# Kernel tuning notes

Hardware: AMD Instinct MI355X
Metric: run time of the kernel (lower is better)

## Reference

```python
import jax, jax.numpy as jnp
import numpy as np

N_HEADS = 16
BLOCK_SIZE = 256


def setup_inputs() -> dict:
    key = jax.random.key(0)
    ks = jax.random.split(key, 5)
    B, T, C = 4, 4096, 1024
    scale = 0.02
    return {
        "x": jax.random.normal(ks[0], (B, T, C), dtype=jnp.float32),
        "Wqkv": jax.random.normal(ks[1], (C, 3 * C), dtype=jnp.float32) * scale,
        "bqkv": jnp.zeros((3 * C,), dtype=jnp.float32),
        "Wout": jax.random.normal(ks[2], (C, C), dtype=jnp.float32) * scale,
        "bout": jnp.zeros((C,), dtype=jnp.float32),
    }


def reference(x, Wqkv, bqkv, Wout, bout):
    B, T, C = x.shape
    H = N_HEADS
    hd = C // H
    bs = BLOCK_SIZE
    nb = T // bs

    qkv = x @ Wqkv + bqkv                     # [B,T,3C]
    qkv = qkv.reshape(B, T, H, 3 * hd).transpose(0, 2, 1, 3)  # [B,H,T,3hd]
    q, k, v = jnp.split(qkv, 3, axis=-1)      # each [B,H,T,hd]

    # block-diagonal local attention: reshape T -> (nb, bs)
    q = q.reshape(B, H, nb, bs, hd)
    k = k.reshape(B, H, nb, bs, hd)
    v = v.reshape(B, H, nb, bs, hd)

    scores = jnp.einsum("bhnqd,bhnkd->bhnqk", q, k) * (hd ** -0.5)
    attn = jax.nn.softmax(scores, axis=-1)
    o = jnp.einsum("bhnqk,bhnkd->bhnqd", attn, v)  # [B,H,nb,bs,hd]

    o = o.reshape(B, H, T, hd).transpose(0, 2, 1, 3).reshape(B, T, C)
    return o @ Wout + bout
```

## Files before the change

### kernel.cpp

```cpp
#include <hip/hip_runtime.h>

typedef unsigned int u32;
typedef unsigned short u16;
typedef short bf16x8 __attribute__((ext_vector_type(8)));
typedef u16 u16x8 __attribute__((ext_vector_type(8)));
typedef float f32x4 __attribute__((ext_vector_type(4)));


__device__ __forceinline__ u16 f2bf(float f) {
  unsigned u = __float_as_uint(f);
  u += 0x7FFFu + ((u >> 16) & 1u);
  return (u16)(u >> 16);
}

typedef const void __attribute__((address_space(1)))* gas_p;
typedef void __attribute__((address_space(3)))* las_p;

__device__ __forceinline__ void async_ld16(const void* g, void* l) {
  __builtin_amdgcn_global_load_lds((gas_p)g, (las_p)l, 16, 0, 0);
}


__global__ __launch_bounds__(256) void k_cvt_bf16(const float* __restrict__ in,
                                                  u16* __restrict__ out, int n8) {
  int i = blockIdx.x * 256 + threadIdx.x;
  if (i >= n8) return;
  const float4* p = (const float4*)in + (size_t)i * 2;
  float4 a = p[0], b = p[1];
  u16x8 o;
  o[0] = f2bf(a.x); o[1] = f2bf(a.y); o[2] = f2bf(a.z); o[3] = f2bf(a.w);
  o[4] = f2bf(b.x); o[5] = f2bf(b.y); o[6] = f2bf(b.z); o[7] = f2bf(b.w);
  *((u16x8*)out + i) = o;
}


__global__ __launch_bounds__(256) void k_transpose_cvt(const float* __restrict__ in,
                                                       u16* __restrict__ out,
                                                       int R, int Ncols) {
  __shared__ u16 t[32][33];
  int tx = threadIdx.x, ty = threadIdx.y;
  int c0 = blockIdx.x * 32, r0 = blockIdx.y * 32;
#pragma unroll
  for (int j = 0; j < 32; j += 8)
    t[ty + j][tx] = f2bf(in[(size_t)(r0 + ty + j) * Ncols + c0 + tx]);
  __syncthreads();
#pragma unroll
  for (int j = 0; j < 32; j += 8)
    out[(size_t)(c0 + ty + j) * R + r0 + tx] = t[tx][ty + j];
}


#define STAGE_A2(h_, src_, dd_) do {                                       \
    const u16* g_ = (src_) + (size_t)(h_) * 128 * KK;                      \
    u16* s_ = lds + (dd_) * 16384 + (((h_) * 128 + w * 16) << 6);          \
    async_ld16(g_, s_);                                                    \
    async_ld16(g_ + 8 * (size_t)KK, s_ + 512);                             \
  } while (0)

#define STAGE_B2(h_, src_, dd_) do {                                       \
    const u16* g_ = (src_) + (size_t)(h_) * 128 * KK;                      \
    u16* s_ = lds + 32768 + (dd_) * 16384 + (((h_) * 128 + w * 16) << 6);  \
    async_ld16(g_, s_);                                                    \
    async_ld16(g_ + 8 * (size_t)KK, s_ + 512);                             \
  } while (0)

#define MQUAD(M0, N0)                                                      \
    _Pragma("unroll") for (int ks = 0; ks < 2; ++ks)                       \
    _Pragma("unroll") for (int mm = 0; mm < 4; ++mm)                       \
    _Pragma("unroll") for (int nn = 0; nn < 2; ++nn)                       \
      acc[(M0) + mm][(N0) + nn] = __builtin_amdgcn_mfma_f32_16x16x32_bf16( \
          a[(M0) + mm][ks], b[(N0) + nn][ks], acc[(M0) + mm][(N0) + nn], 0, 0, 0);

#define TBX(d_, bS_, aS_)                                                  \
  {                                                                        \
    const int doA = (d_) * 16384, doB = 32768 + (d_) * 16384;              \
    _Pragma("unroll") for (int f = 0; f < 4; ++f) {                        \
      a[f][0] = *(const bf16x8*)(lds + doA + rAoff + f * 1024 + c0);       \
      a[f][1] = *(const bf16x8*)(lds + doA + rAoff + f * 1024 + c1);       \
    }                                                                      \
    _Pragma("unroll") for (int f = 0; f < 2; ++f) {                        \
      b[f][0] = *(const bf16x8*)(lds + doB + rBoff + f * 1024 + c0);       \
      b[f][1] = *(const bf16x8*)(lds + doB + rBoff + f * 1024 + c1);       \
    }                                                                      \
    STAGE_B2(0, bS_, (d_) ^ 1);                                            \
    asm volatile("s_waitcnt lgkmcnt(8)");                                  \
    __builtin_amdgcn_s_barrier();                                          \
    asm volatile("s_waitcnt lgkmcnt(0)");                                  \
    __builtin_amdgcn_s_setprio(1);                                         \
    MQUAD(0, 0)                                                            \
    __builtin_amdgcn_s_setprio(0);                                         \
    __builtin_amdgcn_s_barrier();                                          \
    _Pragma("unroll") for (int f = 4; f < 8; ++f) {                        \
      a[f][0] = *(const bf16x8*)(lds + doA + rAoff + f * 1024 + c0);       \
      a[f][1] = *(const bf16x8*)(lds + doA + rAoff + f * 1024 + c1);       \
    }                                                                      \
    STAGE_B2(1, bS_, (d_) ^ 1);                                            \
    __builtin_amdgcn_s_barrier();                                          \
    asm volatile("s_waitcnt lgkmcnt(0)");                                  \
    __builtin_amdgcn_s_setprio(1);                                         \
    MQUAD(4, 0)                                                            \
    __builtin_amdgcn_s_setprio(0);                                         \
    __builtin_amdgcn_s_barrier();                                          \
    _Pragma("unroll") for (int f = 2; f < 4; ++f) {                        \
      b[f][0] = *(const bf16x8*)(lds + doB + rBoff + f * 1024 + c0);       \
      b[f][1] = *(const bf16x8*)(lds + doB + rBoff + f * 1024 + c1);       \
    }                                                                      \
    STAGE_A2(0, aS_, (d_));                                                \
    __builtin_amdgcn_s_barrier();                                          \
    asm volatile("s_waitcnt lgkmcnt(0)");                                  \
    __builtin_amdgcn_s_setprio(1);                                         \
    MQUAD(4, 2)                                                            \
    __builtin_amdgcn_s_setprio(0);                                         \
    __builtin_amdgcn_s_barrier();                                          \
    STAGE_A2(1, aS_, (d_));                                                \
    __builtin_amdgcn_s_setprio(1);                                         \
    MQUAD(0, 2)                                                            \
    __builtin_amdgcn_s_setprio(0);                                         \
    asm volatile("s_waitcnt vmcnt(4)");                                    \
    __builtin_amdgcn_s_barrier();                                          \
  }

#define EPI(PM0, PN0) do {                                                      \
    int ccol0 = (PN0) + wn * 64 + (lane & 15);                                  \
    float bv0 = bias[ccol0], bv1 = bias[ccol0 + 16];                            \
    float bv2 = bias[ccol0 + 32], bv3 = bias[ccol0 + 48];                       \
    size_t crow0 = (size_t)((PM0) + wm * 128 + ((lane >> 4) << 2));             \
    _Pragma("unroll") for (int m = 0; m < 8; ++m)                               \
    _Pragma("unroll") for (int reg = 0; reg < 4; ++reg) {                       \
      size_t ro = (crow0 + m * 16 + reg) * (size_t)N + ccol0;                   \
      float v0 = acc[m][0][reg] + bv0, v1 = acc[m][1][reg] + bv1;               \
      float v2 = acc[m][2][reg] + bv2, v3 = acc[m][3][reg] + bv3;               \
      if (OUT_BF16) {                                                           \
        ((u16*)Cout)[ro] = f2bf(v0); ((u16*)Cout)[ro + 16] = f2bf(v1);          \
        ((u16*)Cout)[ro + 32] = f2bf(v2); ((u16*)Cout)[ro + 48] = f2bf(v3);     \
      } else {                                                                  \
        ((float*)Cout)[ro] = v0; ((float*)Cout)[ro + 16] = v1;                  \
        ((float*)Cout)[ro + 32] = v2; ((float*)Cout)[ro + 48] = v3;             \
      }                                                                         \
    }                                                                           \
  } while (0)

#define TILE_COORD(tt, mm0, nn0) do {                                           \
    int q_ = nwg >> 3, r_ = nwg & 7, x_ = (tt) & 7, loc_ = (tt) >> 3;           \
    int swz_ = (x_ < r_ ? x_ * (q_ + 1) : r_ * (q_ + 1) + (x_ - r_) * q_) + loc_;\
    mm0 = (swz_ / nbn) << 8; nn0 = (swz_ % nbn) << 8;                           \
  } while (0)

#define ZERO_ACC do {                                                           \
    _Pragma("unroll") for (int m = 0; m < 8; ++m)                               \
    _Pragma("unroll") for (int n = 0; n < 4; ++n)                               \
      acc[m][n] = (f32x4){0.f, 0.f, 0.f, 0.f};                                  \
  } while (0)

template <int OUT_BF16, int KK>
__global__ __launch_bounds__(512, 2) void k_gemm8(const u16* __restrict__ A,
                                                  const u16* __restrict__ Bt,
                                                  const float* __restrict__ bias,
                                                  void* __restrict__ Cout,
                                                  int M, int N) {
  extern __shared__ u16 lds[];
  const int NT = KK / 64;

  int nbn = N >> 8, nbm = M >> 8, nwg = nbm * nbn;
  int tid = threadIdx.x;
  int w = tid >> 6, lane = tid & 63;
  int wm = w >> 2, wn = w & 3;

  int rAoff = (wm * 128 + (lane & 15)) << 6;
  int rBoff = (wn * 64 + (lane & 15)) << 6;
  int hi8 = (lane >> 4) << 3, key8 = (lane & 7) << 3;
  int c0 = hi8 ^ key8;
  int c1 = (32 | hi8) ^ key8;
  int rowoff = w * 16 + (lane >> 3);
  int soff = ((lane & 7) ^ (lane >> 3)) << 3;

  bf16x8 a[8][2], b[4][2];
  f32x4 acc[8][4];

  int t = blockIdx.x;
  int m0, n0;
  TILE_COORD(t, m0, n0);
  const u16* pAg = A + (size_t)(m0 + rowoff) * KK + soff;
  const u16* pBg = Bt + (size_t)(n0 + rowoff) * KK + soff;

  STAGE_A2(0, pAg, 0); STAGE_A2(1, pAg, 0);
  STAGE_B2(0, pBg, 0); STAGE_B2(1, pBg, 0);
  STAGE_A2(0, pAg + 64, 1); STAGE_A2(1, pAg + 64, 1);
  asm volatile("s_waitcnt vmcnt(4)");
  __builtin_amdgcn_s_barrier();
  ZERO_ACC;

  for (;;) {
    int tn = t + gridDim.x;
    bool last = tn >= nwg;
    const u16 *pAgN, *pBgN;
    int m0N = m0, n0N = n0;
    if (last) {
      pAgN = pAg; pBgN = pBg;
    } else {
      TILE_COORD(tn, m0N, n0N);
      pAgN = A + (size_t)(m0N + rowoff) * KK + soff;
      pBgN = Bt + (size_t)(n0N + rowoff) * KK + soff;
    }

    for (int k = 0; k < NT; k += 2) {
      const u16* bS1 = pBg + (k + 1) * 64;
      const u16* aS2 = (k + 2 < NT) ? pAg + (k + 2) * 64 : pAgN + (k + 2 - NT) * 64;
      TBX(0, bS1, aS2);
      const u16* bS2 = (k + 2 < NT) ? pBg + (k + 2) * 64 : pBgN + (k + 2 - NT) * 64;
      const u16* aS3 = (k + 3 < NT) ? pAg + (k + 3) * 64 : pAgN + (k + 3 - NT) * 64;
      TBX(1, bS2, aS3);
    }

    EPI(m0, n0);
    if (last) break;
    t = tn; m0 = m0N; n0 = n0N; pAg = pAgN; pBg = pBgN;
    ZERO_ACC;
  }
  asm volatile("s_waitcnt vmcnt(0)");
}


__global__ __launch_bounds__(512, 2) void k_attn2(const u16* __restrict__ qkv,
                                                  u16* __restrict__ o) {
  __shared__ u16 ldsK[256 * 64];
  __shared__ u16 ldsV[64 * 256];

  int bid = blockIdx.x;
  int g = ((bid & 7) << 7) | (bid >> 3);
  int blk = g & 15, h = (g >> 4) & 15, b = g >> 8;

  int tid = threadIdx.x;
  int w = tid >> 6, lane = tid & 63;
  int hgrp = lane >> 4;
  size_t rowb = ((size_t)(b * 4096 + blk * 256)) * 3072 + (size_t)h * 192;

  int qbase = w * 32;
  const u16* qp0 = qkv + rowb + (size_t)(qbase + (lane & 15)) * 3072 + hgrp * 8;
  const u16* qp1 = qp0 + (size_t)16 * 3072;
  bf16x8 qf00 = *(const bf16x8*)(qp0);
  bf16x8 qf01 = *(const bf16x8*)(qp0 + 32);
  bf16x8 qf10 = *(const bf16x8*)(qp1);
  bf16x8 qf11 = *(const bf16x8*)(qp1 + 32);

#pragma unroll
  for (int it = 0; it < 4; ++it) {
    int trow = it * 64 + (tid >> 3);
    const u16* ksrc = qkv + rowb + (size_t)trow * 3072 + 64 +
                      (((lane & 7) ^ (lane >> 3)) << 3);
    async_ld16(ksrc, ldsK + (it * 64 + w * 8) * 64);
    int d0 = (tid & 7) << 3;
    uint4 vv = *(const uint4*)(qkv + rowb + (size_t)trow * 3072 + 128 + d0);
    union { uint4 v; u16 s[8]; } uv;
    uv.v = vv;
#pragma unroll
    for (int j = 0; j < 8; ++j) {
      int d = d0 + j;
      int key = (((d & 7) ^ ((d >> 3) & 7)) & 7) << 4;
      *(u16*)((char*)ldsV + d * 512 + ((2 * trow) ^ key)) = uv.s[j];
    }
  }
  __syncthreads();

  f32x4 acc0[16] = {}, acc1[16] = {};
  int cb = hgrp << 4;
#pragma unroll
  for (int ct = 0; ct < 16; ++ct) {
    int krow = ct * 16 + (lane & 15);
    const char* kb = (const char*)ldsK + krow * 128;
    int key = (krow & 7) << 4;
    bf16x8 k0 = *(const bf16x8*)(kb + (cb ^ key));
    bf16x8 k1 = *(const bf16x8*)(kb + ((64 + cb) ^ key));
    acc0[ct] = __builtin_amdgcn_mfma_f32_16x16x32_bf16(k0, qf00, acc0[ct], 0, 0, 0);
    acc0[ct] = __builtin_amdgcn_mfma_f32_16x16x32_bf16(k1, qf01, acc0[ct], 0, 0, 0);
    acc1[ct] = __builtin_amdgcn_mfma_f32_16x16x32_bf16(k0, qf10, acc1[ct], 0, 0, 0);
    acc1[ct] = __builtin_amdgcn_mfma_f32_16x16x32_bf16(k1, qf11, acc1[ct], 0, 0, 0);
  }

  const float SC = 0.125f * 1.44269504f;
  float rden0, rden1;
  {
    float mx = -1e30f;
#pragma unroll
    for (int ct = 0; ct < 16; ++ct)
#pragma unroll
      for (int rg = 0; rg < 4; ++rg) mx = fmaxf(mx, acc0[ct][rg]);
    mx = fmaxf(mx, __shfl_xor(mx, 16));
    mx = fmaxf(mx, __shfl_xor(mx, 32));
    float s = 0.f;
#pragma unroll
    for (int ct = 0; ct < 16; ++ct)
#pragma unroll
      for (int rg = 0; rg < 4; ++rg) {
        float p = exp2f((acc0[ct][rg] - mx) * SC);
        acc0[ct][rg] = p;
        s += p;
      }
    s += __shfl_xor(s, 16);
    s += __shfl_xor(s, 32);
    rden0 = 1.f / s;
  }
  {
    float mx = -1e30f;
#pragma unroll
    for (int ct = 0; ct < 16; ++ct)
#pragma unroll
      for (int rg = 0; rg < 4; ++rg) mx = fmaxf(mx, acc1[ct][rg]);
    mx = fmaxf(mx, __shfl_xor(mx, 16));
    mx = fmaxf(mx, __shfl_xor(mx, 32));
    float s = 0.f;
#pragma unroll
    for (int ct = 0; ct < 16; ++ct)
#pragma unroll
      for (int rg = 0; rg < 4; ++rg) {
        float p = exp2f((acc1[ct][rg] - mx) * SC);
        acc1[ct][rg] = p;
        s += p;
      }
    s += __shfl_xor(s, 16);
    s += __shfl_xor(s, 32);
    rden1 = 1.f / s;
  }

  int s1 = (lane & 15) + ((lane >> 4) & 1) * 32;
  int s2 = s1 + 16;
  bool lo = (lane < 32);
  bf16x8 pa0[8], pa1[8];
#define PCONV(ACC, PA)                                                      \
  _Pragma("unroll") for (int kt = 0; kt < 8; ++kt) {                        \
    u32 wA0, wB0, wA1, wB1;                                                 \
    asm("v_cvt_pk_bf16_f32 %0, %1, %2" : "=v"(wA0)                          \
        : "v"(ACC[2 * kt][0]), "v"(ACC[2 * kt][1]));                        \
    asm("v_cvt_pk_bf16_f32 %0, %1, %2" : "=v"(wB0)                          \
        : "v"(ACC[2 * kt][2]), "v"(ACC[2 * kt][3]));                        \
    asm("v_cvt_pk_bf16_f32 %0, %1, %2" : "=v"(wA1)                          \
        : "v"(ACC[2 * kt + 1][0]), "v"(ACC[2 * kt + 1][1]));                \
    asm("v_cvt_pk_bf16_f32 %0, %1, %2" : "=v"(wB1)                          \
        : "v"(ACC[2 * kt + 1][2]), "v"(ACC[2 * kt + 1][3]));                \
    u32 t0a = (u32)__shfl((int)wA0, s1), t0b = (u32)__shfl((int)wA1, s1);   \
    u32 t1a = (u32)__shfl((int)wB0, s1), t1b = (u32)__shfl((int)wB1, s1);   \
    u32 t2a = (u32)__shfl((int)wA0, s2), t2b = (u32)__shfl((int)wA1, s2);   \
    u32 t3a = (u32)__shfl((int)wB0, s2), t3b = (u32)__shfl((int)wB1, s2);   \
    union { u32 w[4]; bf16x8 v; } pu;                                       \
    pu.w[0] = lo ? t0a : t0b;                                               \
    pu.w[1] = lo ? t1a : t1b;                                               \
    pu.w[2] = lo ? t2a : t2b;                                               \
    pu.w[3] = lo ? t3a : t3b;                                               \
    PA[kt] = pu.v;                                                          \
  }
  PCONV(acc0, pa0)
  PCONV(acc1, pa1)
#undef PCONV

  f32x4 oa0[4] = {}, oa1[4] = {};
#pragma unroll
  for (int kt = 0; kt < 8; ++kt) {
    int vkb = 2 * (kt * 32 + hgrp * 8);
#pragma unroll
    for (int nt = 0; nt < 4; ++nt) {
      int vd = nt * 16 + (lane & 15);
      int key = (((vd & 7) ^ ((vd >> 3) & 7)) & 7) << 4;
      bf16x8 vf = *(const bf16x8*)((char*)ldsV + vd * 512 + (vkb ^ key));
      oa0[nt] = __builtin_amdgcn_mfma_f32_16x16x32_bf16(pa0[kt], vf, oa0[nt], 0, 0, 0);
      oa1[nt] = __builtin_amdgcn_mfma_f32_16x16x32_bf16(pa1[kt], vf, oa1[nt], 0, 0, 0);
    }
  }

  float rd0[4], rd1[4];
#pragma unroll
  for (int rg = 0; rg < 4; ++rg) {
    rd0[rg] = __shfl(rden0, 4 * hgrp + rg, 16);
    rd1[rg] = __shfl(rden1, 4 * hgrp + rg, 16);
  }
  size_t ob = ((size_t)(b * 4096 + blk * 256 + qbase)) * 1024 + (size_t)h * 64;
#pragma unroll
  for (int nt = 0; nt < 4; ++nt)
#pragma unroll
    for (int rg = 0; rg < 4; ++rg) {
      int col = nt * 16 + (lane & 15);
      o[ob + (size_t)(4 * hgrp + rg) * 1024 + col] = f2bf(oa0[nt][rg] * rd0[rg]);
      o[ob + (size_t)(16 + 4 * hgrp + rg) * 1024 + col] = f2bf(oa1[nt][rg] * rd1[rg]);
    }
}


extern "C" void kernel_launch(void* const* d_in, const int* in_sizes, int n_in,
                              void* d_out, int out_size, void* d_ws, size_t ws_size,
                              hipStream_t stream) {
  (void)in_sizes; (void)n_in; (void)out_size; (void)ws_size;
  const float* x = (const float*)d_in[0];
  const float* Wqkv = (const float*)d_in[1];
  const float* bqkv = (const float*)d_in[2];
  const float* Wout = (const float*)d_in[3];
  const float* bout = (const float*)d_in[4];
  float* out = (float*)d_out;

  char* ws = (char*)d_ws;
  u16* xb    = (u16*)(ws + 0);
  u16* wqkvT = (u16*)(ws + 33554432);
  u16* woT   = (u16*)(ws + 39845888);
  u16* qkv   = (u16*)(ws + 41943040);
  u16* ob    = (u16*)(ws + 142606336);

  hipFuncSetAttribute(reinterpret_cast<const void*>(&k_gemm8<1, 1024>),
                      hipFuncAttributeMaxDynamicSharedMemorySize, 131072);
  hipFuncSetAttribute(reinterpret_cast<const void*>(&k_gemm8<0, 1024>),
                      hipFuncAttributeMaxDynamicSharedMemorySize, 131072);

  k_cvt_bf16<<<8192, 256, 0, stream>>>(x, xb, 16384 * 1024 / 8);
  k_transpose_cvt<<<dim3(96, 32), dim3(32, 8), 0, stream>>>(Wqkv, wqkvT, 1024, 3072);
  k_transpose_cvt<<<dim3(32, 32), dim3(32, 8), 0, stream>>>(Wout, woT, 1024, 1024);

  k_gemm8<1, 1024><<<256, 512, 131072, stream>>>(xb, wqkvT, bqkv, qkv, 16384, 3072);

  k_attn2<<<1024, 512, 0, stream>>>(qkv, ob);

  k_gemm8<0, 1024><<<256, 512, 131072, stream>>>(ob, woT, bout, out, 16384, 1024);
}
```

Baseline: 228.5 us.

## Restructure GEMM main loop to one barrier per phase with cross-barrier fragment prefetch

Replaces the four-barrier-per-half-step GEMM pipeline with a phase that has a single vmcnt(0) wait and barrier. The first A/B fragments of the next LDS buffer are loaded before the last MFMA quad, so LDS reads overlap with compute. Global-to-LDS staging is regrouped so both B halves are issued up front and both A halves after the barrier. The aim is to cut barrier and wait stalls, at the cost of holding more registers live and relying on careful buffer-reuse ordering.

```diff
diff --git a/kernel.cpp b/kernel.cpp
--- a/kernel.cpp
+++ b/kernel.cpp
@@ -65,59 +65,55 @@
   } while (0)
 
 #define MQUAD(M0, N0)                                                      \
+    __builtin_amdgcn_s_setprio(1);                                         \
     _Pragma("unroll") for (int ks = 0; ks < 2; ++ks)                       \
     _Pragma("unroll") for (int mm = 0; mm < 4; ++mm)                       \
     _Pragma("unroll") for (int nn = 0; nn < 2; ++nn)                       \
       acc[(M0) + mm][(N0) + nn] = __builtin_amdgcn_mfma_f32_16x16x32_bf16( \
-          a[(M0) + mm][ks], b[(N0) + nn][ks], acc[(M0) + mm][(N0) + nn], 0, 0, 0);
-
-#define TBX(d_, bS_, aS_)                                                  \
-  {                                                                        \
-    const int doA = (d_) * 16384, doB = 32768 + (d_) * 16384;              \
+          a[(M0) + mm][ks], b[(N0) + nn][ks], acc[(M0) + mm][(N0) + nn], 0, 0, 0); \
+    __builtin_amdgcn_s_setprio(0);
+
+#define RD_A47(dd_)                                                        \
+    _Pragma("unroll") for (int f = 4; f < 8; ++f) {                        \
+      a[f][0] = *(const bf16x8*)(lds + (dd_) * 16384 + rAoff + f * 1024 + c0); \
+      a[f][1] = *(const bf16x8*)(lds + (dd_) * 16384 + rAoff + f * 1024 + c1); \
+    }
+
+#define RD_B23(dd_)                                                        \
+    _Pragma("unroll") for (int f = 2; f < 4; ++f) {                        \
+      b[f][0] = *(const bf16x8*)(lds + 32768 + (dd_) * 16384 + rBoff + f * 1024 + c0); \
+      b[f][1] = *(const bf16x8*)(lds + 32768 + (dd_) * 16384 + rBoff + f * 1024 + c1); \
+    }
+
+#define RD_QA(dd_)                                                         \
     _Pragma("unroll") for (int f = 0; f < 4; ++f) {                        \
-      a[f][0] = *(const bf16x8*)(lds + doA + rAoff + f * 1024 + c0);       \
-      a[f][1] = *(const bf16x8*)(lds + doA + rAoff + f * 1024 + c1);       \
+      a[f][0] = *(const bf16x8*)(lds + (dd_) * 16384 + rAoff + f * 1024 + c0); \
+      a[f][1] = *(const bf16x8*)(lds + (dd_) * 16384 + rAoff + f * 1024 + c1); \
     }                                                                      \
     _Pragma("unroll") for (int f = 0; f < 2; ++f) {                        \
-      b[f][0] = *(const bf16x8*)(lds + doB + rBoff + f * 1024 + c0);       \
-      b[f][1] = *(const bf16x8*)(lds + doB + rBoff + f * 1024 + c1);       \
-    }                                                                      \
+      b[f][0] = *(const bf16x8*)(lds + 32768 + (dd_) * 16384 + rBoff + f * 1024 + c0); \
+      b[f][1] = *(const bf16x8*)(lds + 32768 + (dd_) * 16384 + rBoff + f * 1024 + c1); \
+    }
+
+#define PH(d_, bS_, aS_)                                                   \
+  {                                                                        \
+                                                                   \
+    RD_A47(d_);                                                            \
     STAGE_B2(0, bS_, (d_) ^ 1);                                            \
-    asm volatile("s_waitcnt lgkmcnt(8)");                                  \
+    STAGE_B2(1, bS_, (d_) ^ 1);                                            \
+    MQUAD(0, 0)                                       \
+                                                                   \
+    RD_B23(d_);                                                            \
+    MQUAD(4, 0)                                       \
+                                                                   \
+    MQUAD(0, 2)                                       \
+    asm volatile("s_waitcnt vmcnt(0)" ::: "memory");                       \
     __builtin_amdgcn_s_barrier();                                          \
-    asm volatile("s_waitcnt lgkmcnt(0)");                                  \
-    __builtin_amdgcn_s_setprio(1);                                         \
-    MQUAD(0, 0)                                                            \
-    __builtin_amdgcn_s_setprio(0);                                         \
-    __builtin_amdgcn_s_barrier();                                          \
-    _Pragma("unroll") for (int f = 4; f < 8; ++f) {                        \
-      a[f][0] = *(const bf16x8*)(lds + doA + rAoff + f * 1024 + c0);       \
-      a[f][1] = *(const bf16x8*)(lds + doA + rAoff + f * 1024 + c1);       \
-    }                                                                      \
-    STAGE_B2(1, bS_, (d_) ^ 1);                                            \
-    __builtin_amdgcn_s_barrier();                                          \
-    asm volatile("s_waitcnt lgkmcnt(0)");                                  \
-    __builtin_amdgcn_s_setprio(1);                                         \
-    MQUAD(4, 0)                                                            \
-    __builtin_amdgcn_s_setprio(0);                                         \
-    __builtin_amdgcn_s_barrier();                                          \
-    _Pragma("unroll") for (int f = 2; f < 4; ++f) {                        \
-      b[f][0] = *(const bf16x8*)(lds + doB + rBoff + f * 1024 + c0);       \
-      b[f][1] = *(const bf16x8*)(lds + doB + rBoff + f * 1024 + c1);       \
-    }                                                                      \
-    STAGE_A2(0, aS_, (d_));                                                \
-    __builtin_amdgcn_s_barrier();                                          \
-    asm volatile("s_waitcnt lgkmcnt(0)");                                  \
-    __builtin_amdgcn_s_setprio(1);                                         \
-    MQUAD(4, 2)                                                            \
-    __builtin_amdgcn_s_setprio(0);                                         \
-    __builtin_amdgcn_s_barrier();                                          \
-    STAGE_A2(1, aS_, (d_));                                                \
-    __builtin_amdgcn_s_setprio(1);                                         \
-    MQUAD(0, 2)                                                            \
-    __builtin_amdgcn_s_setprio(0);                                         \
-    asm volatile("s_waitcnt vmcnt(4)");                                    \
-    __builtin_amdgcn_s_barrier();                                          \
+                                                                   \
+    STAGE_A2(0, aS_, d_);                                                  \
+    STAGE_A2(1, aS_, d_);                                                  \
+    RD_QA((d_) ^ 1);                          \
+    MQUAD(4, 2)                                       \
   }
 
 #define EPI(PM0, PN0) do {                                                      \
@@ -186,8 +182,9 @@
   STAGE_A2(0, pAg, 0); STAGE_A2(1, pAg, 0);
   STAGE_B2(0, pBg, 0); STAGE_B2(1, pBg, 0);
   STAGE_A2(0, pAg + 64, 1); STAGE_A2(1, pAg + 64, 1);
-  asm volatile("s_waitcnt vmcnt(4)");
+  asm volatile("s_waitcnt vmcnt(4)" ::: "memory");
   __builtin_amdgcn_s_barrier();
+  RD_QA(0);
   ZERO_ACC;
 
   for (;;) {
@@ -206,10 +203,10 @@
     for (int k = 0; k < NT; k += 2) {
       const u16* bS1 = pBg + (k + 1) * 64;
       const u16* aS2 = (k + 2 < NT) ? pAg + (k + 2) * 64 : pAgN + (k + 2 - NT) * 64;
-      TBX(0, bS1, aS2);
+      PH(0, bS1, aS2)
       const u16* bS2 = (k + 2 < NT) ? pBg + (k + 2) * 64 : pBgN + (k + 2 - NT) * 64;
       const u16* aS3 = (k + 3 < NT) ? pAg + (k + 3) * 64 : pAgN + (k + 3 - NT) * 64;
-      TBX(1, bS2, aS3);
+      PH(1, bS2, aS3)
     }
 
     EPI(m0, n0);
@@ -217,7 +214,7 @@
     t = tn; m0 = m0N; n0 = n0N; pAg = pAgN; pBg = pBgN;
     ZERO_ACC;
   }
-  asm volatile("s_waitcnt vmcnt(0)");
+  asm volatile("s_waitcnt vmcnt(0) lgkmcnt(0)" ::: "memory");
 }
 
 
```

Result: slower. 245.7 us (+7.5%).

## Switch GEMM inner loop from 16x16x32 to 32x32x16 MFMA tiles

Applied to the files above, without the earlier changes.

Rewrites the persistent GEMM's per-wave compute to use 32x32x16 bf16 MFMA instructions instead of 16x16x32, regrouping fragments into 4x2 accumulators of 16 floats with four k-slices per fragment. The LDS read offsets, swizzle column selection and epilogue row/column mapping are rewritten to match the 32x32 output layout. Larger MFMA tiles cut the number of LDS fragment reads and instruction issues per FLOP. The cost is a less coalesced epilogue store pattern and possibly different LDS bank-conflict behaviour.

```diff
diff --git a/kernel.cpp b/kernel.cpp
--- a/kernel.cpp
+++ b/kernel.cpp
@@ -5,6 +5,7 @@
 typedef short bf16x8 __attribute__((ext_vector_type(8)));
 typedef u16 u16x8 __attribute__((ext_vector_type(8)));
 typedef float f32x4 __attribute__((ext_vector_type(4)));
+typedef float f32x16 __attribute__((ext_vector_type(16)));
 
 
 __device__ __forceinline__ u16 f2bf(float f) {
@@ -64,78 +65,67 @@
     async_ld16(g_ + 8 * (size_t)KK, s_ + 512);                             \
   } while (0)
 
-#define MQUAD(M0, N0)                                                      \
-    _Pragma("unroll") for (int ks = 0; ks < 2; ++ks)                       \
-    _Pragma("unroll") for (int mm = 0; mm < 4; ++mm)                       \
-    _Pragma("unroll") for (int nn = 0; nn < 2; ++nn)                       \
-      acc[(M0) + mm][(N0) + nn] = __builtin_amdgcn_mfma_f32_16x16x32_bf16( \
-          a[(M0) + mm][ks], b[(N0) + nn][ks], acc[(M0) + mm][(N0) + nn], 0, 0, 0);
+#define MQ(M0, NB)                                                         \
+    __builtin_amdgcn_s_setprio(1);                                         \
+    _Pragma("unroll") for (int ks = 0; ks < 4; ++ks)                       \
+    _Pragma("unroll") for (int mm = 0; mm < 2; ++mm)                       \
+      acc[(M0) + mm][NB] = __builtin_amdgcn_mfma_f32_32x32x16_bf16(        \
+          a[(M0) + mm][ks], b[NB][ks], acc[(M0) + mm][NB], 0, 0, 0);       \
+    __builtin_amdgcn_s_setprio(0);
 
 #define TBX(d_, bS_, aS_)                                                  \
   {                                                                        \
     const int doA = (d_) * 16384, doB = 32768 + (d_) * 16384;              \
-    _Pragma("unroll") for (int f = 0; f < 4; ++f) {                        \
-      a[f][0] = *(const bf16x8*)(lds + doA + rAoff + f * 1024 + c0);       \
-      a[f][1] = *(const bf16x8*)(lds + doA + rAoff + f * 1024 + c1);       \
-    }                                                                      \
-    _Pragma("unroll") for (int f = 0; f < 2; ++f) {                        \
-      b[f][0] = *(const bf16x8*)(lds + doB + rBoff + f * 1024 + c0);       \
-      b[f][1] = *(const bf16x8*)(lds + doB + rBoff + f * 1024 + c1);       \
+                    \
+    _Pragma("unroll") for (int ks = 0; ks < 4; ++ks) {                     \
+      a[0][ks] = *(const bf16x8*)(lds + doA + rA + 0 * 2048 + c4[ks]);     \
+      a[1][ks] = *(const bf16x8*)(lds + doA + rA + 1 * 2048 + c4[ks]);     \
+      b[0][ks] = *(const bf16x8*)(lds + doB + rB + 0 * 2048 + c4[ks]);     \
     }                                                                      \
     STAGE_B2(0, bS_, (d_) ^ 1);                                            \
     asm volatile("s_waitcnt lgkmcnt(8)");                                  \
     __builtin_amdgcn_s_barrier();                                          \
     asm volatile("s_waitcnt lgkmcnt(0)");                                  \
-    __builtin_amdgcn_s_setprio(1);                                         \
-    MQUAD(0, 0)                                                            \
-    __builtin_amdgcn_s_setprio(0);                                         \
-    __builtin_amdgcn_s_barrier();                                          \
-    _Pragma("unroll") for (int f = 4; f < 8; ++f) {                        \
-      a[f][0] = *(const bf16x8*)(lds + doA + rAoff + f * 1024 + c0);       \
-      a[f][1] = *(const bf16x8*)(lds + doA + rAoff + f * 1024 + c1);       \
+    MQ(0, 0)                                                               \
+    __builtin_amdgcn_s_barrier();                                          \
+                                \
+    _Pragma("unroll") for (int ks = 0; ks < 4; ++ks) {                     \
+      a[2][ks] = *(const bf16x8*)(lds + doA + rA + 2 * 2048 + c4[ks]);     \
+      a[3][ks] = *(const bf16x8*)(lds + doA + rA + 3 * 2048 + c4[ks]);     \
     }                                                                      \
     STAGE_B2(1, bS_, (d_) ^ 1);                                            \
     __builtin_amdgcn_s_barrier();                                          \
     asm volatile("s_waitcnt lgkmcnt(0)");                                  \
-    __builtin_amdgcn_s_setprio(1);                                         \
-    MQUAD(4, 0)                                                            \
-    __builtin_amdgcn_s_setprio(0);                                         \
-    __builtin_amdgcn_s_barrier();                                          \
-    _Pragma("unroll") for (int f = 2; f < 4; ++f) {                        \
-      b[f][0] = *(const bf16x8*)(lds + doB + rBoff + f * 1024 + c0);       \
-      b[f][1] = *(const bf16x8*)(lds + doB + rBoff + f * 1024 + c1);       \
-    }                                                                      \
+    MQ(2, 0)                                                               \
+    __builtin_amdgcn_s_barrier();                                          \
+                                  \
+    _Pragma("unroll") for (int ks = 0; ks < 4; ++ks)                       \
+      b[1][ks] = *(const bf16x8*)(lds + doB + rB + 1 * 2048 + c4[ks]);     \
     STAGE_A2(0, aS_, (d_));                                                \
     __builtin_amdgcn_s_barrier();                                          \
     asm volatile("s_waitcnt lgkmcnt(0)");                                  \
-    __builtin_amdgcn_s_setprio(1);                                         \
-    MQUAD(4, 2)                                                            \
-    __builtin_amdgcn_s_setprio(0);                                         \
-    __builtin_amdgcn_s_barrier();                                          \
+    MQ(2, 1)                                                               \
+    __builtin_amdgcn_s_barrier();                                          \
+                                   \
     STAGE_A2(1, aS_, (d_));                                                \
-    __builtin_amdgcn_s_setprio(1);                                         \
-    MQUAD(0, 2)                                                            \
-    __builtin_amdgcn_s_setprio(0);                                         \
+    MQ(0, 1)                                                               \
     asm volatile("s_waitcnt vmcnt(4)");                                    \
     __builtin_amdgcn_s_barrier();                                          \
   }
 
 #define EPI(PM0, PN0) do {                                                      \
-    int ccol0 = (PN0) + wn * 64 + (lane & 15);                                  \
-    float bv0 = bias[ccol0], bv1 = bias[ccol0 + 16];                            \
-    float bv2 = bias[ccol0 + 32], bv3 = bias[ccol0 + 48];                       \
-    size_t crow0 = (size_t)((PM0) + wm * 128 + ((lane >> 4) << 2));             \
-    _Pragma("unroll") for (int m = 0; m < 8; ++m)                               \
-    _Pragma("unroll") for (int reg = 0; reg < 4; ++reg) {                       \
-      size_t ro = (crow0 + m * 16 + reg) * (size_t)N + ccol0;                   \
-      float v0 = acc[m][0][reg] + bv0, v1 = acc[m][1][reg] + bv1;               \
-      float v2 = acc[m][2][reg] + bv2, v3 = acc[m][3][reg] + bv3;               \
+    int ccolb = (PN0) + wn * 64 + (lane & 31);                                  \
+    float bv0 = bias[ccolb], bv1 = bias[ccolb + 32];                            \
+    int rowb0 = (PM0) + wm * 128 + ((lane >> 5) << 2);                          \
+    _Pragma("unroll") for (int mb = 0; mb < 4; ++mb)                            \
+    _Pragma("unroll") for (int r = 0; r < 16; ++r) {                            \
+      size_t ro = (size_t)(rowb0 + mb * 32 + (r & 3) + ((r >> 2) << 3)) *       \
+                      (size_t)N + ccolb;                                        \
+      float v0 = acc[mb][0][r] + bv0, v1 = acc[mb][1][r] + bv1;                 \
       if (OUT_BF16) {                                                           \
-        ((u16*)Cout)[ro] = f2bf(v0); ((u16*)Cout)[ro + 16] = f2bf(v1);          \
-        ((u16*)Cout)[ro + 32] = f2bf(v2); ((u16*)Cout)[ro + 48] = f2bf(v3);     \
+        ((u16*)Cout)[ro] = f2bf(v0); ((u16*)Cout)[ro + 32] = f2bf(v1);          \
       } else {                                                                  \
-        ((float*)Cout)[ro] = v0; ((float*)Cout)[ro + 16] = v1;                  \
-        ((float*)Cout)[ro + 32] = v2; ((float*)Cout)[ro + 48] = v3;             \
+        ((float*)Cout)[ro] = v0; ((float*)Cout)[ro + 32] = v1;                  \
       }                                                                         \
     }                                                                           \
   } while (0)
@@ -147,9 +137,9 @@
   } while (0)
 
 #define ZERO_ACC do {                                                           \
-    _Pragma("unroll") for (int m = 0; m < 8; ++m)                               \
-    _Pragma("unroll") for (int n = 0; n < 4; ++n)                               \
-      acc[m][n] = (f32x4){0.f, 0.f, 0.f, 0.f};                                  \
+    _Pragma("unroll") for (int m = 0; m < 4; ++m)                               \
+    _Pragma("unroll") for (int n = 0; n < 2; ++n)                               \
+      acc[m][n] = (f32x16)(0.f);                                                \
   } while (0)
 
 template <int OUT_BF16, int KK>
@@ -166,16 +156,18 @@
   int w = tid >> 6, lane = tid & 63;
   int wm = w >> 2, wn = w & 3;
 
-  int rAoff = (wm * 128 + (lane & 15)) << 6;
-  int rBoff = (wn * 64 + (lane & 15)) << 6;
-  int hi8 = (lane >> 4) << 3, key8 = (lane & 7) << 3;
-  int c0 = hi8 ^ key8;
-  int c1 = (32 | hi8) ^ key8;
+  int rA = (wm * 128 + (lane & 31)) << 6;
+  int rB = (wn * 64 + (lane & 31)) << 6;
+  int c4[4];
+#pragma unroll
+  for (int ks = 0; ks < 4; ++ks)
+    c4[ks] = (((2 * ks + (lane >> 5)) ^ (lane & 7)) << 3);
+
   int rowoff = w * 16 + (lane >> 3);
   int soff = ((lane & 7) ^ (lane >> 3)) << 3;
 
-  bf16x8 a[8][2], b[4][2];
-  f32x4 acc[8][4];
+  bf16x8 a[4][4], b[2][4];
+  f32x16 acc[4][2];
 
   int t = blockIdx.x;
   int m0, n0;
@@ -206,10 +198,10 @@
     for (int k = 0; k < NT; k += 2) {
       const u16* bS1 = pBg + (k + 1) * 64;
       const u16* aS2 = (k + 2 < NT) ? pAg + (k + 2) * 64 : pAgN + (k + 2 - NT) * 64;
-      TBX(0, bS1, aS2);
+      TBX(0, bS1, aS2)
       const u16* bS2 = (k + 2 < NT) ? pBg + (k + 2) * 64 : pBgN + (k + 2 - NT) * 64;
       const u16* aS3 = (k + 3 < NT) ? pAg + (k + 3) * 64 : pAgN + (k + 3 - NT) * 64;
-      TBX(1, bS2, aS3);
+      TBX(1, bS2, aS3)
     }
 
     EPI(m0, n0);
@@ -217,7 +209,7 @@
     t = tn; m0 = m0N; n0 = n0N; pAg = pAgN; pBg = pBgN;
     ZERO_ACC;
   }
-  asm volatile("s_waitcnt vmcnt(0)");
+  asm volatile("s_waitcnt vmcnt(0) lgkmcnt(0)");
 }
 
 
```

Result: slower. 240.2 us (+5.1%).

## Split attention blocks into query halves to cut registers and raise occupancy

Applied to the files above, without the earlier changes.

The attention kernel now launches two workgroups per (batch, head, block), each handling 128 query rows with 16 rows per wave instead of 32. This halves the accumulator register footprint, and launch bounds are raised to 4 workgroups per CU. The P conversion is also fused into the PV loop, and V transposition into LDS now packs four rows into 64-bit stores instead of 16-bit scalar stores. The cost is that K and V tiles are loaded and transposed twice, once per half, which doubles that global and LDS traffic.

```diff
diff --git a/kernel.cpp b/kernel.cpp
--- a/kernel.cpp
+++ b/kernel.cpp
@@ -1,6 +1,7 @@
 #include <hip/hip_runtime.h>
 
 typedef unsigned int u32;
+typedef unsigned long long u64;
 typedef unsigned short u16;
 typedef short bf16x8 __attribute__((ext_vector_type(8)));
 typedef u16 u16x8 __attribute__((ext_vector_type(8)));
@@ -206,10 +207,10 @@
     for (int k = 0; k < NT; k += 2) {
       const u16* bS1 = pBg + (k + 1) * 64;
       const u16* aS2 = (k + 2 < NT) ? pAg + (k + 2) * 64 : pAgN + (k + 2 - NT) * 64;
-      TBX(0, bS1, aS2);
+      TBX(0, bS1, aS2)
       const u16* bS2 = (k + 2 < NT) ? pBg + (k + 2) * 64 : pBgN + (k + 2 - NT) * 64;
       const u16* aS3 = (k + 3 < NT) ? pAg + (k + 3) * 64 : pAgN + (k + 3 - NT) * 64;
-      TBX(1, bS2, aS3);
+      TBX(1, bS2, aS3)
     }
 
     EPI(m0, n0);
@@ -217,31 +218,28 @@
     t = tn; m0 = m0N; n0 = n0N; pAg = pAgN; pBg = pBgN;
     ZERO_ACC;
   }
-  asm volatile("s_waitcnt vmcnt(0)");
-}
-
-
-__global__ __launch_bounds__(512, 2) void k_attn2(const u16* __restrict__ qkv,
+  asm volatile("s_waitcnt vmcnt(0) lgkmcnt(0)");
+}
+
+
+__global__ __launch_bounds__(512, 4) void k_attn3(const u16* __restrict__ qkv,
                                                   u16* __restrict__ o) {
   __shared__ u16 ldsK[256 * 64];
   __shared__ u16 ldsV[64 * 256];
 
   int bid = blockIdx.x;
-  int g = ((bid & 7) << 7) | (bid >> 3);
-  int blk = g & 15, h = (g >> 4) & 15, b = g >> 8;
+  int g = ((bid & 7) << 8) | (bid >> 3);
+  int hq = g & 1, blk = (g >> 1) & 15, h = (g >> 5) & 15, b = g >> 9;
 
   int tid = threadIdx.x;
   int w = tid >> 6, lane = tid & 63;
   int hgrp = lane >> 4;
   size_t rowb = ((size_t)(b * 4096 + blk * 256)) * 3072 + (size_t)h * 192;
 
-  int qbase = w * 32;
-  const u16* qp0 = qkv + rowb + (size_t)(qbase + (lane & 15)) * 3072 + hgrp * 8;
-  const u16* qp1 = qp0 + (size_t)16 * 3072;
-  bf16x8 qf00 = *(const bf16x8*)(qp0);
-  bf16x8 qf01 = *(const bf16x8*)(qp0 + 32);
-  bf16x8 qf10 = *(const bf16x8*)(qp1);
-  bf16x8 qf11 = *(const bf16x8*)(qp1 + 32);
+  int qrow = hq * 128 + w * 16 + (lane & 15);
+  const u16* qp = qkv + rowb + (size_t)qrow * 3072 + hgrp * 8;
+  bf16x8 qf0 = *(const bf16x8*)(qp);
+  bf16x8 qf1 = *(const bf16x8*)(qp + 32);
 
 #pragma unroll
   for (int it = 0; it < 4; ++it) {
@@ -249,20 +247,29 @@
     const u16* ksrc = qkv + rowb + (size_t)trow * 3072 + 64 +
                       (((lane & 7) ^ (lane >> 3)) << 3);
     async_ld16(ksrc, ldsK + (it * 64 + w * 8) * 64);
-    int d0 = (tid & 7) << 3;
-    uint4 vv = *(const uint4*)(qkv + rowb + (size_t)trow * 3072 + 128 + d0);
-    union { uint4 v; u16 s[8]; } uv;
-    uv.v = vv;
-#pragma unroll
-    for (int j = 0; j < 8; ++j) {
-      int d = d0 + j;
+  }
+
+  {
+    int tg = tid >> 3, d0 = (tid & 7) << 3;
+    const u16* vsrc = qkv + rowb + (size_t)(4 * tg) * 3072 + 128 + d0;
+    union { uint4 v; u16 s[8]; } r0, r1, r2, r3;
+    r0.v = *(const uint4*)(vsrc);
+    r1.v = *(const uint4*)(vsrc + 3072);
+    r2.v = *(const uint4*)(vsrc + 6144);
+    r3.v = *(const uint4*)(vsrc + 9216);
+    int gb = ((tg >> 1) << 4) + ((tg & 1) << 3);
+#pragma unroll
+    for (int c = 0; c < 8; ++c) {
+      int d = d0 + c;
       int key = (((d & 7) ^ ((d >> 3) & 7)) & 7) << 4;
-      *(u16*)((char*)ldsV + d * 512 + ((2 * trow) ^ key)) = uv.s[j];
+      u64 pack = (u64)r0.s[c] | ((u64)r1.s[c] << 16) |
+                 ((u64)r2.s[c] << 32) | ((u64)r3.s[c] << 48);
+      *(u64*)((char*)ldsV + d * 512 + ((gb & ~15) ^ key) + (gb & 8)) = pack;
     }
   }
   __syncthreads();
 
-  f32x4 acc0[16] = {}, acc1[16] = {};
+  f32x4 acc0[16] = {};
   int cb = hgrp << 4;
 #pragma unroll
   for (int ct = 0; ct < 16; ++ct) {
@@ -271,14 +278,12 @@
     int key = (krow & 7) << 4;
     bf16x8 k0 = *(const bf16x8*)(kb + (cb ^ key));
     bf16x8 k1 = *(const bf16x8*)(kb + ((64 + cb) ^ key));
-    acc0[ct] = __builtin_amdgcn_mfma_f32_16x16x32_bf16(k0, qf00, acc0[ct], 0, 0, 0);
-    acc0[ct] = __builtin_amdgcn_mfma_f32_16x16x32_bf16(k1, qf01, acc0[ct], 0, 0, 0);
-    acc1[ct] = __builtin_amdgcn_mfma_f32_16x16x32_bf16(k0, qf10, acc1[ct], 0, 0, 0);
-    acc1[ct] = __builtin_amdgcn_mfma_f32_16x16x32_bf16(k1, qf11, acc1[ct], 0, 0, 0);
+    acc0[ct] = __builtin_amdgcn_mfma_f32_16x16x32_bf16(k0, qf0, acc0[ct], 0, 0, 0);
+    acc0[ct] = __builtin_amdgcn_mfma_f32_16x16x32_bf16(k1, qf1, acc0[ct], 0, 0, 0);
   }
 
   const float SC = 0.125f * 1.44269504f;
-  float rden0, rden1;
+  float rden0;
   {
     float mx = -1e30f;
 #pragma unroll
@@ -300,86 +305,53 @@
     s += __shfl_xor(s, 32);
     rden0 = 1.f / s;
   }
-  {
-    float mx = -1e30f;
-#pragma unroll
-    for (int ct = 0; ct < 16; ++ct)
-#pragma unroll
-      for (int rg = 0; rg < 4; ++rg) mx = fmaxf(mx, acc1[ct][rg]);
-    mx = fmaxf(mx, __shfl_xor(mx, 16));
-    mx = fmaxf(mx, __shfl_xor(mx, 32));
-    float s = 0.f;
-#pragma unroll
-    for (int ct = 0; ct < 16; ++ct)
-#pragma unroll
-      for (int rg = 0; rg < 4; ++rg) {
-        float p = exp2f((acc1[ct][rg] - mx) * SC);
-        acc1[ct][rg] = p;
-        s += p;
-      }
-    s += __shfl_xor(s, 16);
-    s += __shfl_xor(s, 32);
-    rden1 = 1.f / s;
-  }
 
   int s1 = (lane & 15) + ((lane >> 4) & 1) * 32;
   int s2 = s1 + 16;
   bool lo = (lane < 32);
-  bf16x8 pa0[8], pa1[8];
-#define PCONV(ACC, PA)                                                      \
-  _Pragma("unroll") for (int kt = 0; kt < 8; ++kt) {                        \
-    u32 wA0, wB0, wA1, wB1;                                                 \
-    asm("v_cvt_pk_bf16_f32 %0, %1, %2" : "=v"(wA0)                          \
-        : "v"(ACC[2 * kt][0]), "v"(ACC[2 * kt][1]));                        \
-    asm("v_cvt_pk_bf16_f32 %0, %1, %2" : "=v"(wB0)                          \
-        : "v"(ACC[2 * kt][2]), "v"(ACC[2 * kt][3]));                        \
-    asm("v_cvt_pk_bf16_f32 %0, %1, %2" : "=v"(wA1)                          \
-        : "v"(ACC[2 * kt + 1][0]), "v"(ACC[2 * kt + 1][1]));                \
-    asm("v_cvt_pk_bf16_f32 %0, %1, %2" : "=v"(wB1)                          \
-        : "v"(ACC[2 * kt + 1][2]), "v"(ACC[2 * kt + 1][3]));                \
-    u32 t0a = (u32)__shfl((int)wA0, s1), t0b = (u32)__shfl((int)wA1, s1);   \
-    u32 t1a = (u32)__shfl((int)wB0, s1), t1b = (u32)__shfl((int)wB1, s1);   \
-    u32 t2a = (u32)__shfl((int)wA0, s2), t2b = (u32)__shfl((int)wA1, s2);   \
-    u32 t3a = (u32)__shfl((int)wB0, s2), t3b = (u32)__shfl((int)wB1, s2);   \
-    union { u32 w[4]; bf16x8 v; } pu;                                       \
-    pu.w[0] = lo ? t0a : t0b;                                               \
-    pu.w[1] = lo ? t1a : t1b;                                               \
-    pu.w[2] = lo ? t2a : t2b;                                               \
-    pu.w[3] = lo ? t3a : t3b;                                               \
-    PA[kt] = pu.v;                                                          \
-  }
-  PCONV(acc0, pa0)
-  PCONV(acc1, pa1)
-#undef PCONV
-
-  f32x4 oa0[4] = {}, oa1[4] = {};
+  f32x4 oa[4] = {};
 #pragma unroll
   for (int kt = 0; kt < 8; ++kt) {
+    u32 wA0, wB0, wA1, wB1;
+    asm("v_cvt_pk_bf16_f32 %0, %1, %2" : "=v"(wA0)
+        : "v"(acc0[2 * kt][0]), "v"(acc0[2 * kt][1]));
+    asm("v_cvt_pk_bf16_f32 %0, %1, %2" : "=v"(wB0)
+        : "v"(acc0[2 * kt][2]), "v"(acc0[2 * kt][3]));
+    asm("v_cvt_pk_bf16_f32 %0, %1, %2" : "=v"(wA1)
+        : "v"(acc0[2 * kt + 1][0]), "v"(acc0[2 * kt + 1][1]));
+    asm("v_cvt_pk_bf16_f32 %0, %1, %2" : "=v"(wB1)
+        : "v"(acc0[2 * kt + 1][2]), "v"(acc0[2 * kt + 1][3]));
+    u32 t0a = (u32)__shfl((int)wA0, s1), t0b = (u32)__shfl((int)wA1, s1);
+    u32 t1a = (u32)__shfl((int)wB0, s1), t1b = (u32)__shfl((int)wB1, s1);
+    u32 t2a = (u32)__shfl((int)wA0, s2), t2b = (u32)__shfl((int)wA1, s2);
+    u32 t3a = (u32)__shfl((int)wB0, s2), t3b = (u32)__shfl((int)wB1, s2);
+    union { u32 w[4]; bf16x8 v; } pu;
+    pu.w[0] = lo ? t0a : t0b;
+    pu.w[1] = lo ? t1a : t1b;
+    pu.w[2] = lo ? t2a : t2b;
+    pu.w[3] = lo ? t3a : t3b;
+    bf16x8 pa = pu.v;
     int vkb = 2 * (kt * 32 + hgrp * 8);
 #pragma unroll
     for (int nt = 0; nt < 4; ++nt) {
       int vd = nt * 16 + (lane & 15);
       int key = (((vd & 7) ^ ((vd >> 3) & 7)) & 7) << 4;
       bf16x8 vf = *(const bf16x8*)((char*)ldsV + vd * 512 + (vkb ^ key));
-      oa0[nt] = __builtin_amdgcn_mfma_f32_16x16x32_bf16(pa0[kt], vf, oa0[nt], 0, 0, 0);
-      oa1[nt] = __builtin_amdgcn_mfma_f32_16x16x32_bf16(pa1[kt], vf, oa1[nt], 0, 0, 0);
-    }
-  }
-
-  float rd0[4], rd1[4];
-#pragma unroll
-  for (int rg = 0; rg < 4; ++rg) {
-    rd0[rg] = __shfl(rden0, 4 * hgrp + rg, 16);
-    rd1[rg] = __shfl(rden1, 4 * hgrp + rg, 16);
-  }
-  size_t ob = ((size_t)(b * 4096 + blk * 256 + qbase)) * 1024 + (size_t)h * 64;
+      oa[nt] = __builtin_amdgcn_mfma_f32_16x16x32_bf16(pa, vf, oa[nt], 0, 0, 0);
+    }
+  }
+
+  float rd0[4];
+#pragma unroll
+  for (int rg = 0; rg < 4; ++rg) rd0[rg] = __shfl(rden0, 4 * hgrp + rg, 16);
+  size_t ob = ((size_t)(b * 4096 + blk * 256 + hq * 128 + w * 16)) * 1024 +
+              (size_t)h * 64;
 #pragma unroll
   for (int nt = 0; nt < 4; ++nt)
 #pragma unroll
     for (int rg = 0; rg < 4; ++rg) {
       int col = nt * 16 + (lane & 15);
-      o[ob + (size_t)(4 * hgrp + rg) * 1024 + col] = f2bf(oa0[nt][rg] * rd0[rg]);
-      o[ob + (size_t)(16 + 4 * hgrp + rg) * 1024 + col] = f2bf(oa1[nt][rg] * rd1[rg]);
+      o[ob + (size_t)(4 * hgrp + rg) * 1024 + col] = f2bf(oa[nt][rg] * rd0[rg]);
     }
 }
 
@@ -413,7 +385,7 @@
 
   k_gemm8<1, 1024><<<256, 512, 131072, stream>>>(xb, wqkvT, bqkv, qkv, 16384, 3072);
 
-  k_attn2<<<1024, 512, 0, stream>>>(qkv, ob);
+  k_attn3<<<2048, 512, 0, stream>>>(qkv, ob);
 
   k_gemm8<0, 1024><<<256, 512, 131072, stream>>>(ob, woT, bout, out, 16384, 1024);
 }
```

Measured after the change: 220.7 us. 3.4% less time.
